# Kernel optimization log

Measured on AMD Instinct MI355X. Metric: run time of the kernel, lower is better.

The kernel has to match this reference:

```python
import jax, jax.numpy as jnp
import numpy as np

# Config (Mamba2-2.7B-like)
HID = 2048          # hidden_size
EXPAND = 2
INTER = EXPAND * HID   # 4096
NH = 64             # num_heads
HD = 64             # head_dim (NH*HD == INTER)
NG = 8              # n_groups
SS = 128            # state_size
CK = 4              # conv_kernel
CH = 256            # chunk_size
EPS = 1e-6
CONV_DIM = INTER + 2 * NG * SS          # 6144
PROJ = INTER + CONV_DIM + NH            # 10304
B_SZ, SEQ = 2, 2048


def segment_sum(x):
    # x: [..., T] -> [..., T, T]; stable cumulative-sum based segment sums
    T = x.shape[-1]
    x = jnp.repeat(x[..., None], T, axis=-1)
    x = jnp.where(jnp.tril(jnp.ones((T, T), dtype=bool), k=-1), x, 0.0)
    s = jnp.cumsum(x, axis=-2)
    return jnp.where(jnp.tril(jnp.ones((T, T), dtype=bool), k=0), s, -jnp.inf)


def setup_inputs() -> dict:
    key = jax.random.key(0)
    ks = jax.random.split(key, 6)
    sc = 0.02
    return {
        "input_states": jax.random.normal(ks[0], (B_SZ, SEQ, HID), dtype=jnp.float32),
        "in_proj_w": jax.random.normal(ks[1], (HID, PROJ), dtype=jnp.float32) * sc,
        "conv_w": jax.random.normal(ks[2], (CK, 1, CONV_DIM), dtype=jnp.float32) * sc,  # WIO, depthwise
        "conv_b": jnp.zeros((CONV_DIM,), dtype=jnp.float32),
        "dt_bias": jnp.ones((NH,), dtype=jnp.float32),
        "A_log": jnp.log(jnp.arange(1, NH + 1, dtype=jnp.float32)),
        "D": jnp.ones((NH,), dtype=jnp.float32),
        "norm_w": jnp.ones((INTER,), dtype=jnp.float32),
        "out_proj_w": jax.random.normal(ks[3], (INTER, HID), dtype=jnp.float32) * sc,
    }


def reference(input_states, in_proj_w, conv_w, conv_b, dt_bias, A_log, D, norm_w, out_proj_w):
    b, s, _ = input_states.shape
    proj = input_states @ in_proj_w                                   # [b,s,PROJ]
    gate, hBC, dt = jnp.split(proj, [INTER, INTER + CONV_DIM], axis=-1)

    # depthwise causal-ish conv (flax nn.Conv with padding='SAME', groups=CONV_DIM)
    hBC = jax.lax.conv_general_dilated(
        hBC, conv_w, window_strides=(1,), padding="SAME",
        dimension_numbers=("NWC", "WIO", "NWC"), feature_group_count=CONV_DIM,
    ) + conv_b
    hBC = jax.nn.silu(hBC)[:, :s]
    hs, Bmat, Cmat = jnp.split(hBC, [INTER, INTER + NG * SS], axis=-1)

    A = -jnp.exp(A_log.astype(jnp.float32))                           # [h]
    dt = jax.nn.softplus(dt + dt_bias)                                # [b,s,h]
    dt = jnp.maximum(dt, 0.0)                                         # time_step_limit (0, inf)

    hs = hs.reshape(b, s, NH, HD).astype(jnp.float32)                 # [b,s,h,p]
    Bmat = Bmat.reshape(b, s, NG, SS).astype(jnp.float32)
    Cmat = Cmat.reshape(b, s, NG, SS).astype(jnp.float32)
    Bmat = jnp.repeat(Bmat, NH // NG, axis=2)                         # [b,s,h,n]
    Cmat = jnp.repeat(Cmat, NH // NG, axis=2)

    pad = (CH - s % CH) % CH

    def to_chunks(t):
        t = jnp.pad(t, [(0, 0), (0, pad)] + [(0, 0)] * (t.ndim - 2))
        return t.reshape(b, -1, CH, *t.shape[2:])

    D_res = D[None, None, :, None] * jnp.pad(hs, [(0, 0), (0, pad), (0, 0), (0, 0)])

    hs_dt = hs * dt[..., None]                                        # discretize x
    A_bt = A[None, None, :] * dt                                      # [b,s,h]

    hs_c = to_chunks(hs_dt)                                           # [b,c,l,h,p]
    A_c = to_chunks(A_bt)                                             # [b,c,l,h]
    B_c = to_chunks(Bmat)                                             # [b,c,l,h,n]
    C_c = to_chunks(Cmat)

    A_p = jnp.transpose(A_c, (0, 3, 1, 2))                            # [b,h,c,l]
    A_cum = jnp.cumsum(A_p, axis=-1)

    # 1. intra-chunk (diagonal blocks)
    L = jnp.exp(segment_sum(A_p))                                     # [b,h,c,l,l]
    M = jnp.einsum("bclhn,bcshn->bclsh", C_c, B_c) * jnp.transpose(L, (0, 2, 3, 4, 1))
    Y_diag = jnp.einsum("bclsh,bcshp->bclhp", M, hs_c)

    # 2. intra-chunk states
    decay_states = jnp.exp(A_cum[..., -1:] - A_cum)                   # [b,h,c,l]
    B_decay = B_c * jnp.transpose(decay_states, (0, 2, 3, 1))[..., None]
    states = jnp.einsum("bclhn,bclhp->bchpn", B_decay, hs_c)          # [b,c,h,p,n]

    # 3. inter-chunk recurrence
    states = jnp.concatenate([jnp.zeros_like(states[:, :1]), states], axis=1)  # [b,c+1,h,p,n]
    A_last = jnp.pad(A_cum[..., -1], [(0, 0), (0, 0), (1, 0)])        # [b,h,c+1]
    decay_chunk = jnp.exp(segment_sum(A_last))                        # [b,h,c+1,c+1]
    new_states = jnp.einsum("bhij,bjhpn->bihpn", decay_chunk, states)
    states_out = new_states[:, :-1]                                   # [b,c,h,p,n]

    # 4. state -> output
    state_decay_out = jnp.exp(A_cum)                                  # [b,h,c,l]
    Y_off = jnp.einsum("bclhn,bchpn->bclhp", C_c, states_out) \
        * jnp.transpose(state_decay_out, (0, 2, 3, 1))[..., None]

    y = (Y_diag + Y_off).reshape(b, -1, NH, HD) + D_res
    y = y[:, :s].reshape(b, s, INTER)

    # gated RMSNorm
    yf = y.astype(jnp.float32) * jax.nn.silu(gate.astype(jnp.float32))
    var = jnp.mean(jnp.square(yf), axis=-1, keepdims=True)
    yn = norm_w * (yf * jax.lax.rsqrt(var + EPS))

    return (yn.astype(input_states.dtype)) @ out_proj_w
```

## Files before the change

kernel.cpp:

```cpp
#include <hip/hip_runtime.h>
#include <hip/hip_bf16.h>


#define S_LEN 2048
#define HIDDEN 2048
#define INTER 4096
#define NH 64
#define HD 64
#define NG 8
#define SSZ 128
#define CONV_DIM 6144
#define PROJ_DIM 10304
#define PROJ_PAD 10368
#define NC 8
#define CHK 256
#define ROWS 4096
#define DT_OFF 10240
#define B_OFF 4096
#define C_OFF 5120

typedef __hip_bfloat16 bf16;
typedef __attribute__((ext_vector_type(8))) short bf16x8;
typedef __attribute__((ext_vector_type(4))) float f32x4;
#define MFMA16(a, b, c) __builtin_amdgcn_mfma_f32_16x16x32_bf16(a, b, c, 0, 0, 0)

union U16x8 { uint4 u; bf16x8 v; };

__device__ __forceinline__ float siluf(float x) { return x / (1.f + __expf(-x)); }
__device__ __forceinline__ float ldf(const float* p) { return *p; }
__device__ __forceinline__ float ldf(const bf16* p) { return __bfloat162float(*p); }
__device__ __forceinline__ unsigned short f2bu(float x) {
  bf16 h = __float2bfloat16(x);
  return __builtin_bit_cast(unsigned short, h);
}
__device__ __forceinline__ float bu2f(unsigned short u) {
  return __uint_as_float(((unsigned)u) << 16);
}
__device__ __forceinline__ unsigned pack2(float lo, float hi) {
  return ((unsigned)f2bu(hi) << 16) | f2bu(lo);
}
__device__ __forceinline__ void gload16(const void* g, void* l) {
  __builtin_amdgcn_global_load_lds((const __attribute__((address_space(1))) unsigned*)g,
                                   (__attribute__((address_space(3))) unsigned*)l, 16, 0, 0);
}

__global__ __launch_bounds__(256) void cvt_bf16_k(const float* __restrict__ x,
                                                  unsigned short* __restrict__ o, int n4) {
  int idx = blockIdx.x * 256 + threadIdx.x;
  int stride = gridDim.x * 256;
  for (int i = idx; i < n4; i += stride) {
    float4 v = reinterpret_cast<const float4*>(x)[i];
    uint2 u = make_uint2(pack2(v.x, v.y), pack2(v.z, v.w));
    reinterpret_cast<uint2*>(o)[i] = u;
  }
}

__global__ __launch_bounds__(256) void wT_k(const float* __restrict__ W,
                                            unsigned short* __restrict__ Wt,
                                            int K, int N) {
  __shared__ unsigned short t[64][72];
  int n0 = blockIdx.x * 64, k0 = blockIdx.y * 64;
  int tid = threadIdx.x;
#pragma unroll
  for (int i = 0; i < 16; ++i) {
    int idx = tid + i * 256;
    int kr = idx >> 6, nc = idx & 63;
    float v = (n0 + nc < N) ? W[(size_t)(k0 + kr) * N + n0 + nc] : 0.f;
    t[kr][nc] = f2bu(v);
  }
  __syncthreads();
#pragma unroll
  for (int i = 0; i < 16; ++i) {
    int idx = tid + i * 256;
    int nr = idx >> 6, kc = idx & 63;
    Wt[(size_t)(n0 + nr) * K + k0 + kc] = t[kc][nr];
  }
}

template <int BN, typename TC>
__global__ __launch_bounds__(256) void gemm_bf16(const unsigned short* __restrict__ A,
                                                 const unsigned short* __restrict__ Bt,
                                                 TC* __restrict__ C,
                                                 int M, int N, int K) {
  __shared__ __align__(16) unsigned short sA[128 * 64];
  __shared__ __align__(16) unsigned short sB[BN * 64];
  const int tid = threadIdx.x;
  const int lane = tid & 63, hi = lane >> 4, sl = lane & 15;
  const int wid = tid >> 6, wm = wid >> 1, wn = wid & 1;
  const int gx = gridDim.x;
  int lin = blockIdx.y * gx + blockIdx.x;
  int cpx = (gx * gridDim.y) >> 3;
  int swz = (lin & 7) * cpx + (lin >> 3);
  const int m0 = (swz / gx) * 128;
  const int n0 = (swz % gx) * BN;
  const int lrow = lane >> 3;
  const int lslot = lane & 7;
  constexpr int NCH = 16 + BN / 8;
  constexpr int PER = NCH / 4;
  constexpr int FN = BN / 32;

  f32x4 acc[4][FN] = {};
  for (int kt = 0; kt < K; kt += 64) {
    __syncthreads();
#pragma unroll
    for (int i = 0; i < PER; ++i) {
      int ch = wid * PER + i;
      if (ch < 16) {
        int r = ch * 8 + lrow;
        int g = lslot ^ (r & 7);
        gload16(&A[(size_t)(m0 + r) * K + kt + g * 8], &sA[ch * 512]);
      } else {
        int r = (ch - 16) * 8 + lrow;
        int g = lslot ^ (r & 7);
        gload16(&Bt[(size_t)(n0 + r) * K + kt + g * 8], &sB[(ch - 16) * 512]);
      }
    }
    __syncthreads();
#pragma unroll
    for (int su = 0; su < 2; ++su) {
      bf16x8 af[4], bfr[FN];
#pragma unroll
      for (int m = 0; m < 4; ++m) {
        int r = wm * 64 + m * 16 + sl;
        af[m] = *reinterpret_cast<const bf16x8*>(
            &sA[r * 64 + (((su * 4 + hi) ^ (r & 7)) * 8)]);
      }
#pragma unroll
      for (int j = 0; j < FN; ++j) {
        int r = wn * (BN / 2) + j * 16 + sl;
        bfr[j] = *reinterpret_cast<const bf16x8*>(
            &sB[r * 64 + (((su * 4 + hi) ^ (r & 7)) * 8)]);
      }
#pragma unroll
      for (int m = 0; m < 4; ++m)
#pragma unroll
        for (int j = 0; j < FN; ++j)
          acc[m][j] = MFMA16(af[m], bfr[j], acc[m][j]);
    }
  }
#pragma unroll
  for (int m = 0; m < 4; ++m)
#pragma unroll
    for (int j = 0; j < FN; ++j) {
      int col = n0 + wn * (BN / 2) + j * 16 + sl;
      if (col < N) {
#pragma unroll
        for (int r = 0; r < 4; ++r) {
          int row = m0 + wm * 64 + m * 16 + hi * 4 + r;
          if constexpr (sizeof(TC) == 2)
            C[(size_t)row * N + col] = __float2bfloat16(acc[m][j][r]);
          else
            C[(size_t)row * N + col] = acc[m][j][r];
        }
      }
    }
}

__global__ __launch_bounds__(256) void conv_silu_k(const bf16* __restrict__ proj,
                                                   const float* __restrict__ cw,
                                                   const float* __restrict__ cb,
                                                   bf16* __restrict__ convo) {
  int idx = blockIdx.x * 256 + threadIdx.x;
  int ci = idx % (CONV_DIM / 8);
  int row = idx / (CONV_DIM / 8);
  int c8 = ci * 8;
  int t = row & (S_LEN - 1);
  int b = row >> 11;
  float acc[8];
  {
    float4 b0 = *reinterpret_cast<const float4*>(&cb[c8]);
    float4 b1 = *reinterpret_cast<const float4*>(&cb[c8 + 4]);
    acc[0] = b0.x; acc[1] = b0.y; acc[2] = b0.z; acc[3] = b0.w;
    acc[4] = b1.x; acc[5] = b1.y; acc[6] = b1.z; acc[7] = b1.w;
  }
#pragma unroll
  for (int w = 0; w < 4; w++) {
    int tt = t + w - 1;
    if (tt >= 0 && tt < S_LEN) {
      U16x8 u;
      u.u = *reinterpret_cast<const uint4*>(
          &proj[(size_t)(b * S_LEN + tt) * PROJ_DIM + INTER + c8]);
      float4 w0 = *reinterpret_cast<const float4*>(&cw[w * CONV_DIM + c8]);
      float4 w1 = *reinterpret_cast<const float4*>(&cw[w * CONV_DIM + c8 + 4]);
      acc[0] += w0.x * bu2f((unsigned short)u.v[0]);
      acc[1] += w0.y * bu2f((unsigned short)u.v[1]);
      acc[2] += w0.z * bu2f((unsigned short)u.v[2]);
      acc[3] += w0.w * bu2f((unsigned short)u.v[3]);
      acc[4] += w1.x * bu2f((unsigned short)u.v[4]);
      acc[5] += w1.y * bu2f((unsigned short)u.v[5]);
      acc[6] += w1.z * bu2f((unsigned short)u.v[6]);
      acc[7] += w1.w * bu2f((unsigned short)u.v[7]);
    }
  }
  uint4 o;
  o.x = pack2(siluf(acc[0]), siluf(acc[1]));
  o.y = pack2(siluf(acc[2]), siluf(acc[3]));
  o.z = pack2(siluf(acc[4]), siluf(acc[5]));
  o.w = pack2(siluf(acc[6]), siluf(acc[7]));
  *reinterpret_cast<uint4*>(&convo[(size_t)row * CONV_DIM + c8]) = o;
}

__global__ __launch_bounds__(256) void dt_k(const bf16* __restrict__ proj,
                                            const float* __restrict__ dtb,
                                            float* __restrict__ dtp) {
  int idx = blockIdx.x * 256 + threadIdx.x;
  int h = idx & 63;
  int row = idx >> 6;
  float x = ldf(&proj[(size_t)row * PROJ_DIM + DT_OFF + h]) + dtb[h];
  dtp[idx] = (x > 20.f) ? x : log1pf(__expf(x));
}

__global__ __launch_bounds__(256) void acum_k(const float* __restrict__ dtp,
                                              const float* __restrict__ alog,
                                              float* __restrict__ acum) {
  __shared__ float buf[2][CHK];
  int blk = blockIdx.x;
  int c = blk & 7;
  int h = (blk >> 3) & 63;
  int b = blk >> 9;
  int tid = threadIdx.x;
  int row0 = b * S_LEN + c * CHK;
  float a = -__expf(alog[h]);
  buf[0][tid] = a * dtp[(size_t)(row0 + tid) * NH + h];
  __syncthreads();
  int cur = 0;
#pragma unroll
  for (int off = 1; off < 256; off <<= 1) {
    float nv = buf[cur][tid];
    if (tid >= off) nv += buf[cur][tid - off];
    buf[cur ^ 1][tid] = nv;
    cur ^= 1;
    __syncthreads();
  }
  acum[(size_t)blk * CHK + tid] = buf[cur][tid];
}

__global__ __launch_bounds__(256) void chunk_states_mfma(const bf16* __restrict__ convo,
                                                         const float* __restrict__ dtp,
                                                         const float* __restrict__ acum,
                                                         float* __restrict__ cs) {
  __shared__ float sAc[CHK];
  __shared__ float sDtf[CHK];
  __shared__ float sEx[64];
  __shared__ __align__(16) unsigned short sHT[64 * 64];
  __shared__ __align__(16) unsigned short sBd[128 * 64];
  const int tid = threadIdx.x;
  const int lane = tid & 63, hi = lane >> 4, sl = lane & 15;
  const int wid = tid >> 6, wm = wid >> 1, wn = wid & 1;
  const int blk = blockIdx.x;
  const int h = blk & 63, bc = blk >> 6, c = bc & 7, b = bc >> 3, g = h >> 3;
  const int row0 = b * S_LEN + c * CHK;
  sAc[tid] = acum[((size_t)((b * NH + h) * NC + c)) * CHK + tid];
  sDtf[tid] = dtp[(size_t)(row0 + tid) * NH + h];
  f32x4 acc[2][4] = {};
  for (int ts = 0; ts < 4; ++ts) {
    __syncthreads();
    if (tid < 64) sEx[tid] = __expf(sAc[CHK - 1] - sAc[ts * 64 + tid]);
    __syncthreads();
#pragma unroll
    for (int it = 0; it < 2; ++it) {
      int cid = tid + it * 256;
      int t = cid >> 3, p8 = (cid & 7) * 8;
      U16x8 u;
      u.u = *reinterpret_cast<const uint4*>(
          &convo[(size_t)(row0 + ts * 64 + t) * CONV_DIM + h * HD + p8]);
      float dtv = sDtf[ts * 64 + t];
#pragma unroll
      for (int e = 0; e < 8; ++e) {
        int p = p8 + e;
        int G = (p & 7) ^ ((p >> 3) & 7);
        sHT[p * 64 + (((t >> 3) ^ G) * 8) + (t & 7)] =
            f2bu(bu2f((unsigned short)u.v[e]) * dtv);
      }
    }
#pragma unroll
    for (int it = 0; it < 4; ++it) {
      int cid = tid + it * 256;
      int t = cid >> 4, n8 = (cid & 15) * 8;
      U16x8 u;
      u.u = *reinterpret_cast<const uint4*>(
          &convo[(size_t)(row0 + ts * 64 + t) * CONV_DIM + B_OFF + g * SSZ + n8]);
      float ex = sEx[t];
#pragma unroll
      for (int e = 0; e < 8; ++e) {
        int n = n8 + e;
        int G = (n & 7) ^ ((n >> 3) & 7);
        sBd[n * 64 + (((t >> 3) ^ G) * 8) + (t & 7)] =
            f2bu(bu2f((unsigned short)u.v[e]) * ex);
      }
    }
    __syncthreads();
#pragma unroll
    for (int kc = 0; kc < 2; ++kc) {
      bf16x8 a[2], bb[4];
#pragma unroll
      for (int m = 0; m < 2; ++m) {
        int p = wm * 32 + m * 16 + sl;
        int G = (p & 7) ^ ((p >> 3) & 7);
        a[m] = *reinterpret_cast<const bf16x8*>(
            &sHT[p * 64 + (((kc * 4 + hi) ^ G) * 8)]);
      }
#pragma unroll
      for (int j = 0; j < 4; ++j) {
        int n = wn * 64 + j * 16 + sl;
        int G = (n & 7) ^ ((n >> 3) & 7);
        bb[j] = *reinterpret_cast<const bf16x8*>(
            &sBd[n * 64 + (((kc * 4 + hi) ^ G) * 8)]);
      }
#pragma unroll
      for (int m = 0; m < 2; ++m)
#pragma unroll
        for (int j = 0; j < 4; ++j) acc[m][j] = MFMA16(a[m], bb[j], acc[m][j]);
    }
  }
  size_t base = (size_t)blk * HD * SSZ;
#pragma unroll
  for (int m = 0; m < 2; ++m)
#pragma unroll
    for (int j = 0; j < 4; ++j)
#pragma unroll
      for (int r = 0; r < 4; ++r) {
        int p = wm * 32 + m * 16 + hi * 4 + r;
        int n = wn * 64 + j * 16 + sl;
        cs[base + (size_t)p * SSZ + n] = acc[m][j][r];
      }
}

__global__ __launch_bounds__(256) void chunk_rec_k(const float* __restrict__ acum,
                                                   float* __restrict__ cs) {
  int idx = blockIdx.x * 256 + threadIdx.x;
  int n = idx & 127;
  int p = (idx >> 7) & 63;
  int h = (idx >> 13) & 63;
  int b = idx >> 19;
  float run = 0.f;
#pragma unroll
  for (int c = 0; c < NC; c++) {
    size_t off = ((size_t)(((b * NC + c) * NH + h) * HD + p)) * SSZ + n;
    float csv = cs[off];
    float al = acum[((size_t)((b * NH + h) * NC + c)) * CHK + (CHK - 1)];
    cs[off] = run;
    run = run * __expf(al) + csv;
  }
}

__global__ __launch_bounds__(256) void chunk_out_mfma(const bf16* __restrict__ convo,
                                                      const float* __restrict__ dtp,
                                                      const float* __restrict__ acum,
                                                      const float* __restrict__ cs,
                                                      const float* __restrict__ Dp,
                                                      bf16* __restrict__ yb) {
  __shared__ float sAc[CHK];
  __shared__ float sDt[CHK];
  __shared__ __align__(16) unsigned short sB[64 * 128];
  __shared__ __align__(16) unsigned short sH[64 * 64];
  __shared__ __align__(16) unsigned short sW[4 * 64 * 64];
  const int tid = threadIdx.x;
  const int lane = tid & 63, hi = lane >> 4, sl = lane & 15;
  const int wid = tid >> 6;
  const int blk = blockIdx.x;
  const int h = blk & 63;
  const int bc = blk >> 6;
  const int c = bc & 7;
  const int b = bc >> 3;
  const int g = h >> 3;
  const int row0 = b * S_LEN + c * CHK;
  unsigned short* sWp = &sW[wid * 4096];

  sAc[tid] = acum[((size_t)((b * NH + h) * NC + c)) * CHK + tid];
  sDt[tid] = dtp[(size_t)(row0 + tid) * NH + h];

  bf16x8 cf[4][4];
#pragma unroll
  for (int m = 0; m < 4; ++m)
#pragma unroll
    for (int kc = 0; kc < 4; ++kc) {
      int l = wid * 64 + m * 16 + sl;
      U16x8 u;
      u.u = *reinterpret_cast<const uint4*>(
          &convo[(size_t)(row0 + l) * CONV_DIM + C_OFF + g * SSZ + kc * 32 + hi * 8]);
      cf[m][kc] = u.v;
    }

  f32x4 acc[4][4] = {};

  for (int st = 0; st < 4; ++st) {
    __syncthreads();
#pragma unroll
    for (int it = 0; it < 4; ++it) {
      int cid = tid + it * 256;
      int s = cid >> 4, gr = cid & 15;
      const uint4* p = reinterpret_cast<const uint4*>(
          &convo[(size_t)(row0 + st * 64 + s) * CONV_DIM + B_OFF + g * SSZ + gr * 8]);
      *reinterpret_cast<uint4*>(&sB[s * 128 + (gr ^ (s & 7)) * 8]) = *p;
    }
#pragma unroll
    for (int it = 0; it < 16; ++it) {
      int cid = tid + it * 256;
      int s = cid >> 6, pp = cid & 63;
      float v = ldf(&convo[(size_t)(row0 + st * 64 + s) * CONV_DIM + h * HD + pp]) *
                sDt[st * 64 + s];
      sH[pp * 64 + (((s >> 3) ^ (pp & 7)) * 8) + (s & 7)] = f2bu(v);
    }
    __syncthreads();
    if (wid >= st) {
#pragma unroll
      for (int sf = 0; sf < 4; ++sf) {
        f32x4 d[4] = {};
#pragma unroll
        for (int kc = 0; kc < 4; ++kc) {
          int srow = sf * 16 + sl;
          bf16x8 bfv = *reinterpret_cast<const bf16x8*>(
              &sB[srow * 128 + (((kc * 4 + hi) ^ (srow & 7)) * 8)]);
#pragma unroll
          for (int m = 0; m < 4; ++m) d[m] = MFMA16(cf[m][kc], bfv, d[m]);
        }
        int s_loc = sf * 16 + sl;
        int s_glob = st * 64 + s_loc;
        float acS = sAc[s_glob];
        bool diag = (st == wid);
#pragma unroll
        for (int m = 0; m < 4; ++m)
#pragma unroll
          for (int r = 0; r < 4; ++r) {
            int l_loc = m * 16 + hi * 4 + r;
            int l_glob = wid * 64 + l_loc;
            float e = __expf(sAc[l_glob] - acS);
            float v = d[m][r] * e;
            if (diag && s_glob > l_glob) v = 0.f;
            sWp[l_loc * 64 + (((s_loc >> 3) ^ (l_loc & 7)) * 8) + (s_loc & 7)] = f2bu(v);
          }
      }
    }
    __syncthreads();
    if (wid >= st) {
#pragma unroll
      for (int kc = 0; kc < 2; ++kc) {
        bf16x8 a[4], bb[4];
#pragma unroll
        for (int m = 0; m < 4; ++m) {
          int l = m * 16 + sl;
          a[m] = *reinterpret_cast<const bf16x8*>(
              &sWp[l * 64 + (((kc * 4 + hi) ^ (l & 7)) * 8)]);
        }
#pragma unroll
        for (int j = 0; j < 4; ++j) {
          int p = j * 16 + sl;
          bb[j] = *reinterpret_cast<const bf16x8*>(
              &sH[p * 64 + (((kc * 4 + hi) ^ (p & 7)) * 8)]);
        }
#pragma unroll
        for (int m = 0; m < 4; ++m)
#pragma unroll
          for (int j = 0; j < 4; ++j) acc[m][j] = MFMA16(a[m], bb[j], acc[m][j]);
      }
    }
  }

  __syncthreads();
  {
    size_t sinbase = ((size_t)(((b * NC + c) * NH + h) * HD)) * SSZ;
#pragma unroll
    for (int it = 0; it < 8; ++it) {
      int cid = tid + it * 256;
      int p = cid >> 5, q = cid & 31;
      float4 v = *reinterpret_cast<const float4*>(&cs[sinbase + (size_t)p * SSZ + q * 4]);
      uint2 val = make_uint2(pack2(v.x, v.y), pack2(v.z, v.w));
      *reinterpret_cast<uint2*>(&sB[p * 128 + ((q >> 1) ^ (p & 7)) * 8 + (q & 1) * 4]) = val;
    }
  }
  __syncthreads();
#pragma unroll
  for (int m = 0; m < 4; ++m) {
    float e = __expf(sAc[wid * 64 + m * 16 + sl]);
#pragma unroll
    for (int kc = 0; kc < 4; ++kc) {
      bf16x8 fv = cf[m][kc];
#pragma unroll
      for (int ei = 0; ei < 8; ++ei) {
        unsigned short us = (unsigned short)fv[ei];
        fv[ei] = (short)f2bu(bu2f(us) * e);
      }
      cf[m][kc] = fv;
    }
  }
#pragma unroll
  for (int kc = 0; kc < 4; ++kc) {
    bf16x8 bb[4];
#pragma unroll
    for (int j = 0; j < 4; ++j) {
      int p = j * 16 + sl;
      bb[j] = *reinterpret_cast<const bf16x8*>(
          &sB[p * 128 + (((kc * 4 + hi) ^ (p & 7)) * 8)]);
    }
#pragma unroll
    for (int m = 0; m < 4; ++m)
#pragma unroll
      for (int j = 0; j < 4; ++j) acc[m][j] = MFMA16(cf[m][kc], bb[j], acc[m][j]);
  }

  float Dh = Dp[h];
#pragma unroll
  for (int m = 0; m < 4; ++m)
#pragma unroll
    for (int j = 0; j < 4; ++j)
#pragma unroll
      for (int r = 0; r < 4; ++r) {
        int l_glob = wid * 64 + m * 16 + hi * 4 + r;
        size_t row = (size_t)(row0 + l_glob);
        int pg = j * 16 + sl;
        float hraw = ldf(&convo[row * CONV_DIM + h * HD + pg]);
        yb[row * INTER + h * HD + pg] = __float2bfloat16(acc[m][j][r] + Dh * hraw);
      }
}

__global__ __launch_bounds__(256) void norm_k(const bf16* __restrict__ proj,
                                              const float* __restrict__ nw,
                                              bf16* __restrict__ yb) {
  int row = blockIdx.x;
  int tid = threadIdx.x;
  float vals[16];
  float ss = 0.f;
#pragma unroll
  for (int half = 0; half < 2; half++) {
    int colb = tid * 8 + half * 2048;
    U16x8 gy, gg;
    gy.u = *reinterpret_cast<const uint4*>(&yb[(size_t)row * INTER + colb]);
    gg.u = *reinterpret_cast<const uint4*>(&proj[(size_t)row * PROJ_DIM + colb]);
#pragma unroll
    for (int e = 0; e < 8; e++) {
      float yf = bu2f((unsigned short)gy.v[e]) * siluf(bu2f((unsigned short)gg.v[e]));
      vals[half * 8 + e] = yf;
      ss += yf * yf;
    }
  }
#pragma unroll
  for (int off = 32; off > 0; off >>= 1) ss += __shfl_down(ss, off);
  __shared__ float red[4];
  if ((tid & 63) == 0) red[tid >> 6] = ss;
  __syncthreads();
  float tot = red[0] + red[1] + red[2] + red[3];
  float scale = rsqrtf(tot * (1.f / INTER) + 1e-6f);
#pragma unroll
  for (int half = 0; half < 2; half++) {
    int colb = tid * 8 + half * 2048;
    float4 w0 = *reinterpret_cast<const float4*>(&nw[colb]);
    float4 w1 = *reinterpret_cast<const float4*>(&nw[colb + 4]);
    float s0 = vals[half * 8 + 0] * scale * w0.x, s1 = vals[half * 8 + 1] * scale * w0.y;
    float s2 = vals[half * 8 + 2] * scale * w0.z, s3 = vals[half * 8 + 3] * scale * w0.w;
    float s4 = vals[half * 8 + 4] * scale * w1.x, s5 = vals[half * 8 + 5] * scale * w1.y;
    float s6 = vals[half * 8 + 6] * scale * w1.z, s7 = vals[half * 8 + 7] * scale * w1.w;
    uint4 o = make_uint4(pack2(s0, s1), pack2(s2, s3), pack2(s4, s5), pack2(s6, s7));
    *reinterpret_cast<uint4*>(&yb[(size_t)row * INTER + colb]) = o;
  }
}

extern "C" void kernel_launch(void* const* d_in, const int* in_sizes, int n_in,
                              void* d_out, int out_size, void* d_ws, size_t ws_size,
                              hipStream_t stream) {
  const float* x     = (const float*)d_in[0];
  const float* wproj = (const float*)d_in[1];
  const float* cw    = (const float*)d_in[2];
  const float* cb    = (const float*)d_in[3];
  const float* dtb   = (const float*)d_in[4];
  const float* alog  = (const float*)d_in[5];
  const float* Dp    = (const float*)d_in[6];
  const float* nw    = (const float*)d_in[7];
  const float* wout  = (const float*)d_in[8];
  float* out = (float*)d_out;
  char* ws = (char*)d_ws;

  bf16*  proj  = (bf16*)(ws);
  bf16*  convo = (bf16*)(ws + 84410368);
  bf16*  yb    = (bf16*)(ws + 134742016);
  float* dtp   = (float*)(ws + 168296448);
  float* acum  = (float*)(ws + 169345024);
  float* cs    = (float*)(ws + 170393600);
  unsigned short* Wt1 = (unsigned short*)(ws + 84410368);
  unsigned short* xb  = (unsigned short*)(ws + 134742016);
  unsigned short* Wt2 = (unsigned short*)(ws + 170393600);

  cvt_bf16_k<<<dim3(2048), 256, 0, stream>>>(x, xb, ROWS * HIDDEN / 4);
  wT_k<<<dim3(PROJ_PAD / 64, HIDDEN / 64), 256, 0, stream>>>(wproj, Wt1, HIDDEN, PROJ_DIM);
  gemm_bf16<128, bf16><<<dim3(PROJ_PAD / 128, ROWS / 128), 256, 0, stream>>>(
      xb, Wt1, proj, ROWS, PROJ_DIM, HIDDEN);
  conv_silu_k<<<dim3(ROWS * CONV_DIM / 8 / 256), 256, 0, stream>>>(proj, cw, cb, convo);
  dt_k<<<dim3(ROWS * NH / 256), 256, 0, stream>>>(proj, dtb, dtp);
  acum_k<<<dim3(2 * NH * NC), 256, 0, stream>>>(dtp, alog, acum);
  chunk_states_mfma<<<dim3(2 * NC * NH), 256, 0, stream>>>(convo, dtp, acum, cs);
  chunk_rec_k<<<dim3(2 * NH * HD * SSZ / 256), 256, 0, stream>>>(acum, cs);
  chunk_out_mfma<<<dim3(2 * NC * NH), 256, 0, stream>>>(convo, dtp, acum, cs, Dp, yb);
  norm_k<<<dim3(ROWS), 256, 0, stream>>>(proj, nw, yb);
  wT_k<<<dim3(HIDDEN / 64, INTER / 64), 256, 0, stream>>>(wout, Wt2, INTER, HIDDEN);
  gemm_bf16<64, float><<<dim3(HIDDEN / 64, ROWS / 128), 256, 0, stream>>>(
      (const unsigned short*)yb, Wt2, out, ROWS, HIDDEN, INTER);
}
```

Before: 567.9 us.

## Replace in-projection GEMM with 256x256 tile, 9-slot LDS pipelined MFMA kernel

Adds a new 512-thread GEMM that computes 256x256 output tiles. It stages A and B half-tiles through a 9-slot ring buffer in dynamic LDS (144 KB), interleaving global loads with MFMA phases and using s_setprio and scheduling barriers to overlap memory with compute. The goal is to cut the input-projection GEMM time by raising data reuse per tile and hiding load latency. PROJ_PAD is raised so N divides by 256, which means padded work plus more weight transpose and workspace footprint. The large LDS use limits occupancy, and the assumed workspace layout may now be tight.

Result: faster. 515.0 us (-9.3%).

```diff
diff --git a/kernel.cpp b/kernel.cpp
--- a/kernel.cpp
+++ b/kernel.cpp
@@ -11,7 +11,7 @@
 #define SSZ 128
 #define CONV_DIM 6144
 #define PROJ_DIM 10304
-#define PROJ_PAD 10368
+#define PROJ_PAD 10496
 #define NC 8
 #define CHK 256
 #define ROWS 4096
@@ -75,6 +75,163 @@
     int nr = idx >> 6, kc = idx & 63;
     Wt[(size_t)(n0 + nr) * K + k0 + kc] = t[kc][nr];
   }
+}
+
+__device__ __forceinline__ int mod9(int x) { return x >= 9 ? x - 9 : x; }
+
+__device__ __forceinline__ void stage_half(const unsigned short* __restrict__ A,
+                                           const unsigned short* __restrict__ Bt,
+                                           unsigned short* lds9, int hj, int slot,
+                                           int m0, int n0, int K, int hmax,
+                                           int tid, int wid) {
+  if (hj >= hmax) return;
+  const int t = hj >> 2, i = hj & 3;
+  const unsigned short* src = (i < 2) ? A : Bt;
+  const int br = ((i < 2) ? m0 : n0) + (i & 1) * 128;
+  const int g = (tid & 7) ^ ((tid >> 3) & 7);
+#pragma unroll
+  for (int r = 0; r < 2; ++r) {
+    int row = r * 64 + (tid >> 3);
+    gload16(&src[(size_t)(br + row) * K + t * 64 + g * 8],
+            &lds9[slot * 8192 + r * 4096 + wid * 512]);
+  }
+}
+
+template <typename TC>
+__global__ __launch_bounds__(512, 2) void gemm_8ph(const unsigned short* __restrict__ A,
+                                                   const unsigned short* __restrict__ Bt,
+                                                   TC* __restrict__ C,
+                                                   int M, int N, int K) {
+  extern __shared__ unsigned short lds9[];
+  const int tid = threadIdx.x;
+  const int lane = tid & 63, hi = lane >> 4, sl = lane & 15;
+  const int wid = tid >> 6;
+  const int wm = wid >> 2, wn = wid & 3;
+  const int gx = gridDim.x;
+  int lin = blockIdx.y * gx + blockIdx.x;
+  int cpx = (gx * gridDim.y) >> 3;
+  int swz = (lin & 7) * cpx + (lin >> 3);
+  const int m0 = (swz / gx) * 256;
+  const int n0 = (swz % gx) * 256;
+  const int NT = K >> 6;
+  const int HMAX = NT << 2;
+  const int rbB = (wn & 1) * 64;
+
+  f32x4 acc[8][4] = {};
+  bf16x8 a0[4][2], a1[4][2], bb[4][2];
+
+#pragma unroll
+  for (int j = 0; j < 5; ++j)
+    stage_half(A, Bt, lds9, j, j, m0, n0, K, HMAX, tid, wid);
+
+  int j0 = 0;
+  for (int t = 0; t < NT; ++t) {
+    const int sAw = mod9(j0 + wm);
+    const int sBw = mod9(j0 + 2 + (wn >> 1));
+    asm volatile("s_waitcnt vmcnt(2)" ::: "memory");
+    __builtin_amdgcn_sched_barrier(0);
+    __builtin_amdgcn_s_barrier();
+    __builtin_amdgcn_sched_barrier(0);
+#pragma unroll
+    for (int mf = 0; mf < 4; ++mf)
+#pragma unroll
+      for (int kk = 0; kk < 2; ++kk) {
+        int ra = mf * 16 + sl;
+        a0[mf][kk] = *reinterpret_cast<const bf16x8*>(
+            &lds9[sAw * 8192 + ra * 64 + (((kk * 4 + hi) ^ (ra & 7)) * 8)]);
+      }
+#pragma unroll
+    for (int nf = 0; nf < 2; ++nf)
+#pragma unroll
+      for (int kk = 0; kk < 2; ++kk) {
+        int rb = rbB + nf * 16 + sl;
+        bb[nf][kk] = *reinterpret_cast<const bf16x8*>(
+            &lds9[sBw * 8192 + rb * 64 + (((kk * 4 + hi) ^ (rb & 7)) * 8)]);
+      }
+    stage_half(A, Bt, lds9, 4 * t + 5, mod9(j0 + 5), m0, n0, K, HMAX, tid, wid);
+    asm volatile("s_waitcnt lgkmcnt(0)" ::: "memory");
+    __builtin_amdgcn_sched_barrier(0);
+    __builtin_amdgcn_s_setprio(1);
+#pragma unroll
+    for (int mf = 0; mf < 4; ++mf)
+#pragma unroll
+      for (int nf = 0; nf < 2; ++nf)
+#pragma unroll
+        for (int kk = 0; kk < 2; ++kk)
+          acc[mf][nf] = MFMA16(a0[mf][kk], bb[nf][kk], acc[mf][nf]);
+    __builtin_amdgcn_s_setprio(0);
+    __builtin_amdgcn_sched_barrier(0);
+#pragma unroll
+    for (int nf = 2; nf < 4; ++nf)
+#pragma unroll
+      for (int kk = 0; kk < 2; ++kk) {
+        int rb = rbB + nf * 16 + sl;
+        bb[nf][kk] = *reinterpret_cast<const bf16x8*>(
+            &lds9[sBw * 8192 + rb * 64 + (((kk * 4 + hi) ^ (rb & 7)) * 8)]);
+      }
+    stage_half(A, Bt, lds9, 4 * t + 6, mod9(j0 + 6), m0, n0, K, HMAX, tid, wid);
+    asm volatile("s_waitcnt lgkmcnt(0)" ::: "memory");
+    __builtin_amdgcn_sched_barrier(0);
+    __builtin_amdgcn_s_setprio(1);
+#pragma unroll
+    for (int mf = 0; mf < 4; ++mf)
+#pragma unroll
+      for (int nf = 2; nf < 4; ++nf)
+#pragma unroll
+        for (int kk = 0; kk < 2; ++kk)
+          acc[mf][nf] = MFMA16(a0[mf][kk], bb[nf][kk], acc[mf][nf]);
+    __builtin_amdgcn_s_setprio(0);
+    __builtin_amdgcn_sched_barrier(0);
+#pragma unroll
+    for (int mf = 0; mf < 4; ++mf)
+#pragma unroll
+      for (int kk = 0; kk < 2; ++kk) {
+        int ra = (mf + 4) * 16 + sl;
+        a1[mf][kk] = *reinterpret_cast<const bf16x8*>(
+            &lds9[sAw * 8192 + ra * 64 + (((kk * 4 + hi) ^ (ra & 7)) * 8)]);
+      }
+    stage_half(A, Bt, lds9, 4 * t + 7, mod9(j0 + 7), m0, n0, K, HMAX, tid, wid);
+    asm volatile("s_waitcnt lgkmcnt(0)" ::: "memory");
+    __builtin_amdgcn_sched_barrier(0);
+    __builtin_amdgcn_s_setprio(1);
+#pragma unroll
+    for (int mf = 0; mf < 4; ++mf)
+#pragma unroll
+      for (int nf = 0; nf < 2; ++nf)
+#pragma unroll
+        for (int kk = 0; kk < 2; ++kk)
+          acc[mf + 4][nf] = MFMA16(a1[mf][kk], bb[nf][kk], acc[mf + 4][nf]);
+    __builtin_amdgcn_s_setprio(0);
+    __builtin_amdgcn_sched_barrier(0);
+    stage_half(A, Bt, lds9, 4 * t + 8, mod9(j0 + 8), m0, n0, K, HMAX, tid, wid);
+    __builtin_amdgcn_s_setprio(1);
+#pragma unroll
+    for (int mf = 0; mf < 4; ++mf)
+#pragma unroll
+      for (int nf = 2; nf < 4; ++nf)
+#pragma unroll
+        for (int kk = 0; kk < 2; ++kk)
+          acc[mf + 4][nf] = MFMA16(a1[mf][kk], bb[nf][kk], acc[mf + 4][nf]);
+    __builtin_amdgcn_s_setprio(0);
+    __builtin_amdgcn_sched_barrier(0);
+    j0 += 4; if (j0 >= 9) j0 -= 9;
+  }
+#pragma unroll
+  for (int mf = 0; mf < 8; ++mf)
+#pragma unroll
+    for (int nf = 0; nf < 4; ++nf) {
+      int col = n0 + wn * 64 + nf * 16 + sl;
+      if (col < N) {
+#pragma unroll
+        for (int r = 0; r < 4; ++r) {
+          int row = m0 + wm * 128 + mf * 16 + hi * 4 + r;
+          if constexpr (sizeof(TC) == 2)
+            C[(size_t)row * N + col] = __float2bfloat16(acc[mf][nf][r]);
+          else
+            C[(size_t)row * N + col] = acc[mf][nf][r];
+        }
+      }
+    }
 }
 
 template <int BN, typename TC>
@@ -580,9 +737,12 @@
   unsigned short* xb  = (unsigned short*)(ws + 134742016);
   unsigned short* Wt2 = (unsigned short*)(ws + 170393600);
 
+  hipFuncSetAttribute(reinterpret_cast<const void*>(&gemm_8ph<bf16>),
+                      hipFuncAttributeMaxDynamicSharedMemorySize, 147456);
+
   cvt_bf16_k<<<dim3(2048), 256, 0, stream>>>(x, xb, ROWS * HIDDEN / 4);
   wT_k<<<dim3(PROJ_PAD / 64, HIDDEN / 64), 256, 0, stream>>>(wproj, Wt1, HIDDEN, PROJ_DIM);
-  gemm_bf16<128, bf16><<<dim3(PROJ_PAD / 128, ROWS / 128), 256, 0, stream>>>(
+  gemm_8ph<bf16><<<dim3(PROJ_PAD / 256, ROWS / 256), 512, 147456, stream>>>(
       xb, Wt1, proj, ROWS, PROJ_DIM, HIDDEN);
   conv_silu_k<<<dim3(ROWS * CONV_DIM / 8 / 256), 256, 0, stream>>>(proj, cw, cb, convo);
   dt_k<<<dim3(ROWS * NH / 256), 256, 0, stream>>>(proj, dtb, dtp);
```
